# Kernel tuning notes

Measured on AMD Instinct MI355X. Metric: run time of the kernel, lower is better.

## Reference

```python
import jax, jax.numpy as jnp
import numpy as np

D_MODEL = 1024
D_Q = 1024
D_K = 1024
D_V = 1024
B, S = 4, 2048


def setup_inputs() -> dict:
    key = jax.random.key(0)
    kx, kq, kk, kv = jax.random.split(key, 4)
    # torch Linear(in, out) weight is [out, in]; y = x @ W.T. Use kaiming-ish scale.
    sc = 1.0 / np.sqrt(D_MODEL)
    x = jax.random.normal(kx, (B, S, D_MODEL), dtype=jnp.float32)
    Wq = jax.random.normal(kq, (D_Q, D_MODEL), dtype=jnp.float32) * sc
    Wk = jax.random.normal(kk, (D_K, D_MODEL), dtype=jnp.float32) * sc
    Wv = jax.random.normal(kv, (D_V, D_MODEL), dtype=jnp.float32) * sc
    return {"x": x, "Wq": Wq, "Wk": Wk, "Wv": Wv}


def reference(x, Wq, Wk, Wv):
    d_k = Wk.shape[0]
    q = jnp.einsum('bsd,qd->bsq', x, Wq)  # [B,S,d_q]
    k = jnp.einsum('bsd,kd->bsk', x, Wk)  # [B,S,d_k]
    v = jnp.einsum('bsd,vd->bsv', x, Wv)  # [B,S,d_v]
    scores = jnp.einsum('bqd,bkd->bqk', q, k) / jnp.sqrt(jnp.float32(d_k))
    seq = scores.shape[-1]
    causal = jnp.tril(jnp.ones((seq, seq), dtype=bool))  # True = keep
    scores = jnp.where(causal[None, :, :], scores, -jnp.inf)
    probs = jax.nn.softmax(scores, axis=-1)
    return jnp.einsum('bqk,bkv->bqv', probs, v)
```

## Files before the change

kernel.cpp:

```cpp
#include <hip/hip_runtime.h>
#include <hip/hip_bf16.h>
#include <stdint.h>

typedef __attribute__((ext_vector_type(8))) short short8;
typedef __attribute__((ext_vector_type(4))) float floatx4;

typedef const __attribute__((address_space(1))) void* gvp;
typedef __attribute__((address_space(3))) void* lvp;

__device__ __forceinline__ unsigned short f2bf(float f) {
    unsigned u = __float_as_uint(f);
    u += 0x7fffu + ((u >> 16) & 1u);
    return (unsigned short)(u >> 16);
}

#define BAR()   do { asm volatile("" ::: "memory"); __builtin_amdgcn_s_barrier(); asm volatile("" ::: "memory"); } while (0)
#define WAITL() do { asm volatile("s_waitcnt lgkmcnt(0)" ::: "memory"); __builtin_amdgcn_sched_barrier(0); } while (0)
#define WAITV4() asm volatile("s_waitcnt vmcnt(4)" ::: "memory")
#define WAITV0() asm volatile("s_waitcnt vmcnt(0)" ::: "memory")

__global__ __launch_bounds__(256)
void cvt_all(const float* __restrict__ x, const float* __restrict__ wq,
             const float* __restrict__ wk, const float* __restrict__ wv,
             unsigned short* __restrict__ Xb, unsigned short* __restrict__ WqT,
             unsigned short* __restrict__ WkT, unsigned short* __restrict__ Wvb) {
    const int b = blockIdx.x, t = threadIdx.x;
    if (b < 2304) {
        const float* in; unsigned short* out; long base;
        if (b < 2048) { in = x;  out = Xb;  base = (long)b * 1024; }
        else          { in = wv; out = Wvb; base = (long)(b - 2048) * 1024; }
        #pragma unroll
        for (int k = 0; k < 4; ++k) {
            long idx = base + k * 256 + t;
            float4 v = reinterpret_cast<const float4*>(in)[idx];
            uint2 o;
            o.x = (unsigned)f2bf(v.x) | ((unsigned)f2bf(v.y) << 16);
            o.y = (unsigned)f2bf(v.z) | ((unsigned)f2bf(v.w) << 16);
            reinterpret_cast<uint2*>(out)[idx] = o;
        }
    } else {
        const int bb = b - 2304;
        const float* in = (bb < 256) ? wq : wk;
        unsigned short* out = (bb < 256) ? WqT : WkT;
        const int tile = bb & 255;
        const int e0 = (tile >> 4) * 64, d0 = (tile & 15) * 64;
        __shared__ unsigned short ldsT[64][68];
        const int r = t >> 4, cq = t & 15;
        #pragma unroll
        for (int p = 0; p < 4; ++p) {
            const int e = p * 16 + r;
            float4 v = *reinterpret_cast<const float4*>(in + (long)(e0 + e) * 1024 + d0 + cq * 4);
            ldsT[cq*4+0][e] = f2bf(v.x);
            ldsT[cq*4+1][e] = f2bf(v.y);
            ldsT[cq*4+2][e] = f2bf(v.z);
            ldsT[cq*4+3][e] = f2bf(v.w);
        }
        __syncthreads();
        #pragma unroll
        for (int p = 0; p < 4; ++p) {
            const int d = p * 16 + r;
            ushort4 o = *reinterpret_cast<const ushort4*>(&ldsT[d][cq * 4]);
            *reinterpret_cast<ushort4*>(out + (long)(d0 + d) * 1024 + e0 + cq * 4) = o;
        }
    }
}

__device__ __forceinline__ void stage_half(char* slot, const unsigned short* src,
                                           int ld, int k0, int tid) {
    #pragma unroll
    for (int r = 0; r < 2; ++r) {
        const int c = r * 512 + tid;
        const int row = c >> 3;
        const int cs = ((c & 7) * 16) ^ ((row & 7) << 4);
        const char* g = reinterpret_cast<const char*>(src + (long)row * ld + k0) + cs;
        __builtin_amdgcn_global_load_lds((gvp)g,
            (lvp)(slot + r * 8192 + (tid >> 6) * 1024), 16, 0, 0);
    }
}

__device__ __forceinline__ void load_a4(short8 a_[4][2], const char* slot, int mh,
                                        int fr, int csw0, int csw1) {
    #pragma unroll
    for (int i = 0; i < 4; ++i) {
        const int rb = (mh * 64 + i * 16 + fr) * 128;
        a_[i][0] = *reinterpret_cast<const short8*>(slot + rb + csw0);
        a_[i][1] = *reinterpret_cast<const short8*>(slot + rb + csw1);
    }
}

__device__ __forceinline__ void load_b2(short8 b_[2][2], const char* slot, int rbase,
                                        int nh, int fr, int csw0, int csw1) {
    #pragma unroll
    for (int j = 0; j < 2; ++j) {
        const int rb = (rbase + nh * 32 + j * 16 + fr) * 128;
        b_[j][0] = *reinterpret_cast<const short8*>(slot + rb + csw0);
        b_[j][1] = *reinterpret_cast<const short8*>(slot + rb + csw1);
    }
}

__device__ __forceinline__ void mfma16(floatx4 acc[8][4], short8 a_[4][2],
                                       short8 b_[2][2], int mh, int nh) {
    __builtin_amdgcn_s_setprio(1);
    #pragma unroll
    for (int i = 0; i < 4; ++i)
        #pragma unroll
        for (int j = 0; j < 2; ++j) {
            acc[mh*4+i][nh*2+j] = __builtin_amdgcn_mfma_f32_16x16x32_bf16(
                a_[i][0], b_[j][0], acc[mh*4+i][nh*2+j], 0, 0, 0);
            acc[mh*4+i][nh*2+j] = __builtin_amdgcn_mfma_f32_16x16x32_bf16(
                a_[i][1], b_[j][1], acc[mh*4+i][nh*2+j], 0, 0, 0);
        }
    __builtin_amdgcn_s_setprio(0);
}

template<typename CT, int MODE>
__global__ __launch_bounds__(512, 2)
void gemm8p(const unsigned short* __restrict__ A, const unsigned short* B,
            const unsigned short* B1, CT* __restrict__ C, unsigned short* __restrict__ Vt,
            int K, int lda, int ldb, int ldc,
            long sA, long sB, long sC, int nwg)
{
    const int gx = gridDim.x, gy = gridDim.y;
    int flat = (blockIdx.z * gy + blockIdx.y) * gx + blockIdx.x;
    {
        int xcd = flat & 7, lid = flat >> 3;
        int q = nwg >> 3, r = nwg & 7;
        flat = (xcd < r ? xcd * (q + 1) : r * (q + 1) + (xcd - r) * q) + lid;
    }
    int bx, by, bz = 0;
    bool isV = false;
    if (MODE == 1) {
        bx = flat % gx;
        int t2 = flat / gx;
        by = t2 % gy;
        bz = t2 / gy;
        if (bx > by) return;
    } else {
        if (flat >= 128) { isV = true; flat -= 128; B = B1; }
        by = flat >> 2;
        bx = flat & 3;
    }

    A += (long)bz * sA + (long)by * 256 * lda;
    B += (long)bz * sB + (long)bx * 256 * ldb;
    C += (long)bz * sC;

    __shared__ __align__(16) char lds[8 * 16384];
    #define SLOT(db, op, half) (lds + ((((db) << 1 | (op)) << 1 | (half)) * 16384))

    const int tid  = threadIdx.x;
    const int lane = tid & 63;
    const int wid  = tid >> 6;
    const int wm = wid >> 2;
    const int wn = wid & 3;
    const int bh = wn >> 1;
    const int brbase = (wn & 1) * 64;
    const int fr = lane & 15;
    const int csw0 = ((lane >> 4) * 16) ^ ((fr & 7) << 4);
    const int csw1 = (64 + (lane >> 4) * 16) ^ ((fr & 7) << 4);

    const unsigned short* Ah[2] = { A, A + 128ll * lda };
    const unsigned short* Bh[2] = { B, B + 128ll * ldb };

    const int NT = K >> 6;
    const int NI = NT >> 1;

    floatx4 acc[8][4] = {};
    short8 a_[4][2];
    short8 b_[2][2][2];

    stage_half(SLOT(0,1,0), Bh[0], ldb, 0, tid);
    stage_half(SLOT(0,1,1), Bh[1], ldb, 0, tid);
    stage_half(SLOT(0,0,0), Ah[0], lda, 0, tid);
    stage_half(SLOT(0,0,1), Ah[1], lda, 0, tid);
    stage_half(SLOT(1,1,0), Bh[0], ldb, 64, tid);
    stage_half(SLOT(1,1,1), Bh[1], ldb, 64, tid);
    WAITV4();
    BAR();

    for (int I = 0; I < NI; ++I) {
        const int kA1 = min(2*I + 1, NT - 1) * 64;
        const int kT2 = min(2*I + 2, NT - 1) * 64;
        const int kB3 = min(2*I + 3, NT - 1) * 64;

        load_a4(a_, SLOT(0,0,wm), 0, fr, csw0, csw1);
        load_b2(b_[0], SLOT(0,1,bh), brbase, 0, fr, csw0, csw1);
        stage_half(SLOT(1,0,0), Ah[0], lda, kA1, tid);
        BAR(); WAITL();
        mfma16(acc, a_, b_[0], 0, 0);
        BAR();

        load_b2(b_[1], SLOT(0,1,bh), brbase, 1, fr, csw0, csw1);
        stage_half(SLOT(1,0,1), Ah[1], lda, kA1, tid);
        BAR(); WAITL();
        mfma16(acc, a_, b_[1], 0, 1);
        BAR();

        load_a4(a_, SLOT(0,0,wm), 1, fr, csw0, csw1);
        stage_half(SLOT(0,1,0), Bh[0], ldb, kT2, tid);
        BAR(); WAITL();
        mfma16(acc, a_, b_[1], 1, 1);
        BAR();

        stage_half(SLOT(0,1,1), Bh[1], ldb, kT2, tid);
        BAR(); WAITL();
        mfma16(acc, a_, b_[0], 1, 0);
        WAITV4();
        BAR();

        load_a4(a_, SLOT(1,0,wm), 0, fr, csw0, csw1);
        load_b2(b_[0], SLOT(1,1,bh), brbase, 0, fr, csw0, csw1);
        stage_half(SLOT(0,0,0), Ah[0], lda, kT2, tid);
        BAR(); WAITL();
        mfma16(acc, a_, b_[0], 0, 0);
        BAR();

        load_b2(b_[1], SLOT(1,1,bh), brbase, 1, fr, csw0, csw1);
        stage_half(SLOT(0,0,1), Ah[1], lda, kT2, tid);
        BAR(); WAITL();
        mfma16(acc, a_, b_[1], 0, 1);
        BAR();

        load_a4(a_, SLOT(1,0,wm), 1, fr, csw0, csw1);
        stage_half(SLOT(1,1,0), Bh[0], ldb, kB3, tid);
        BAR(); WAITL();
        mfma16(acc, a_, b_[1], 1, 1);
        BAR();

        stage_half(SLOT(1,1,1), Bh[1], ldb, kB3, tid);
        BAR(); WAITL();
        mfma16(acc, a_, b_[0], 1, 0);
        WAITV4();
        BAR();
    }

    if (MODE == 3 && isV) {
        WAITV0();
        BAR();
        char* T = lds;
        #pragma unroll
        for (int i = 0; i < 8; ++i)
            #pragma unroll
            for (int j = 0; j < 4; ++j) {
                const int n = wn * 64 + j * 16 + fr;
                const int m = wm * 128 + ((lane >> 4) << 2) + i * 16;
                uint2 pk;
                pk.x = (unsigned)f2bf(acc[i][j][0]) | ((unsigned)f2bf(acc[i][j][1]) << 16);
                pk.y = (unsigned)f2bf(acc[i][j][2]) | ((unsigned)f2bf(acc[i][j][3]) << 16);
                *reinterpret_cast<uint2*>(T + n * 512 + ((m * 2) ^ ((n & 7) << 4))) = pk;
            }
        __syncthreads();
        const int b  = by >> 3;
        const int s0 = (by & 7) * 256;
        #pragma unroll
        for (int c = 0; c < 16; ++c) {
            const int idx = c * 512 + tid;
            const int n = idx >> 5, k = idx & 31;
            uint4 v = *reinterpret_cast<const uint4*>(T + n * 512 + ((k * 16) ^ ((n & 7) << 4)));
            *reinterpret_cast<uint4*>(Vt + (long)b * (1024 * 2048)
                + (long)(bx * 256 + n) * 2048 + s0 + k * 8) = v;
        }
        return;
    }

    const int cr0 = by * 256 + wm * 128 + (lane >> 4) * 4;
    const int cc0 = bx * 256 + wn * 64 + (lane & 15);
    #pragma unroll
    for (int i = 0; i < 8; ++i)
        #pragma unroll
        for (int j = 0; j < 4; ++j)
            #pragma unroll
            for (int r = 0; r < 4; ++r) {
                long idx = (long)(cr0 + i * 16 + r) * ldc + (cc0 + j * 16);
                float v = acc[i][j][r];
                if constexpr (sizeof(CT) == 4) C[idx] = v;
                else                           C[idx] = (CT)f2bf(v);
            }
    #undef SLOT
}

template<typename CT, int MODE>
__global__ __launch_bounds__(256, 3)
void gemm_bt(const unsigned short* __restrict__ A, const unsigned short* __restrict__ B,
             CT* __restrict__ C, int K, int lda, int ldb, int ldc,
             long sA, long sB, long sC, int nwg, float csc)
{
    const int gx = gridDim.x, gy = gridDim.y;
    int flat = (blockIdx.z * gy + blockIdx.y) * gx + blockIdx.x;
    {
        int xcd = flat & 7, lid = flat >> 3;
        int q = nwg >> 3, r = nwg & 7;
        flat = (xcd < r ? xcd * (q + 1) : r * (q + 1) + (xcd - r) * q) + lid;
    }
    int bx = flat % gx;
    int t2 = flat / gx;
    int by = t2 % gy;
    const int bz = t2 / gy;
    if (MODE == 2) {
        by = ((by & 1) << 3) | ((by & 2) << 1) | ((by & 4) >> 1) | ((by & 8) >> 3);
    }

    A += (long)bz * sA; B += (long)bz * sB; C += (long)bz * sC;
    const int kend = (MODE == 2) ? min(K, (by + 1) * 128) : K;

    __shared__ unsigned short As[128 * 64];
    __shared__ unsigned short Bs[128 * 64];

    const int tid  = threadIdx.x;
    const int lane = tid & 63;
    const int wid  = tid >> 6;
    const int m0 = by * 128, n0 = bx * 128;
    const int wm = (wid >> 1) * 64, wn = (wid & 1) * 64;
    const int frow = lane & 15;
    const int fk   = (lane >> 4) * 8;

    const int srow = lane >> 3;
    const int scolb = (lane & 7) * 16;

    floatx4 acc[4][4] = {};

    for (int k0 = 0; k0 < kend; k0 += 64) {
        __syncthreads();
        #pragma unroll
        for (int i = 0; i < 4; ++i) {
            const int c = wid * 4 + i;
            const int row = c * 8 + srow;
            const char* ga = reinterpret_cast<const char*>(A + (long)(m0 + row) * lda + k0) + scolb;
            __builtin_amdgcn_global_load_lds((gvp)ga,
                (lvp)(reinterpret_cast<char*>(As) + c * 1024), 16, 0, 0);
            const char* gb = reinterpret_cast<const char*>(B + (long)(n0 + row) * ldb + k0) + scolb;
            __builtin_amdgcn_global_load_lds((gvp)gb,
                (lvp)(reinterpret_cast<char*>(Bs) + c * 1024), 16, 0, 0);
        }
        __syncthreads();
        #pragma unroll
        for (int ks = 0; ks < 2; ++ks) {
            short8 af[4], bf[4];
            #pragma unroll
            for (int i = 0; i < 4; ++i) {
                const int ar = wm + i * 16 + frow;
                af[i] = *reinterpret_cast<const short8*>(
                    reinterpret_cast<const char*>(As) + ar * 128 + (ks * 32 + fk) * 2);
                const int br = wn + i * 16 + frow;
                bf[i] = *reinterpret_cast<const short8*>(
                    reinterpret_cast<const char*>(Bs) + br * 128 + (ks * 32 + fk) * 2);
            }
            #pragma unroll
            for (int i = 0; i < 4; ++i)
                #pragma unroll
                for (int j = 0; j < 4; ++j)
                    acc[i][j] = __builtin_amdgcn_mfma_f32_16x16x32_bf16(af[i], bf[j], acc[i][j], 0, 0, 0);
        }
    }

    const int cr0 = m0 + wm + (lane >> 4) * 4;
    const int cc0 = n0 + wn + (lane & 15);
    #pragma unroll
    for (int i = 0; i < 4; ++i)
        #pragma unroll
        for (int j = 0; j < 4; ++j)
            #pragma unroll
            for (int r = 0; r < 4; ++r) {
                long idx = (long)(cr0 + i * 16 + r) * ldc + (cc0 + j * 16);
                float v = acc[i][j][r] * csc;
                if constexpr (sizeof(CT) == 4) C[idx] = v;
                else                           C[idx] = (CT)f2bf(v);
            }
}

__global__ __launch_bounds__(256)
void softmax_causal(float* __restrict__ Sc) {
    const int q = blockIdx.x;
    const int b = blockIdx.y;
    float* row = Sc + ((long)b * 2048 + q) * 2048;
    const int t = threadIdx.x;
    const int lane = t & 63, wid = t >> 6;
    const int kend = (q | 127) + 1;

    float vals[8];
    float mx = -INFINITY;
    #pragma unroll
    for (int i = 0; i < 2; ++i) {
        const int c0 = i * 1024 + t * 4;
        if (c0 <= q) {
            float4 v = *reinterpret_cast<const float4*>(row + c0);
            float tmp[4] = {v.x, v.y, v.z, v.w};
            #pragma unroll
            for (int j = 0; j < 4; ++j) {
                float val = (c0 + j <= q) ? tmp[j] : -INFINITY;
                vals[i * 4 + j] = val;
                mx = fmaxf(mx, val);
            }
        } else {
            vals[i*4+0] = vals[i*4+1] = vals[i*4+2] = vals[i*4+3] = -INFINITY;
        }
    }
    #pragma unroll
    for (int o = 32; o > 0; o >>= 1) mx = fmaxf(mx, __shfl_xor(mx, o));
    __shared__ float rmax[4], rsum[4];
    if (lane == 0) rmax[wid] = mx;
    __syncthreads();
    mx = fmaxf(fmaxf(rmax[0], rmax[1]), fmaxf(rmax[2], rmax[3]));

    float s = 0.f;
    #pragma unroll
    for (int k = 0; k < 8; ++k) {
        float e = __expf(vals[k] - mx);
        vals[k] = e;
        s += e;
    }
    #pragma unroll
    for (int o = 32; o > 0; o >>= 1) s += __shfl_xor(s, o);
    if (lane == 0) rsum[wid] = s;
    __syncthreads();
    s = rsum[0] + rsum[1] + rsum[2] + rsum[3];
    const float inv = 1.f / s;

    unsigned short* orow = reinterpret_cast<unsigned short*>(row);
    #pragma unroll
    for (int i = 0; i < 2; ++i) {
        const int c0 = i * 1024 + t * 4;
        if (c0 < kend) {
            uint2 o;
            o.x = (unsigned)f2bf(vals[i*4+0] * inv) | ((unsigned)f2bf(vals[i*4+1] * inv) << 16);
            o.y = (unsigned)f2bf(vals[i*4+2] * inv) | ((unsigned)f2bf(vals[i*4+3] * inv) << 16);
            *reinterpret_cast<uint2*>(orow + c0) = o;
        }
    }
}

extern "C" void kernel_launch(void* const* d_in, const int* in_sizes, int n_in,
                              void* d_out, int out_size, void* d_ws, size_t ws_size,
                              hipStream_t stream) {
    const float* x  = (const float*)d_in[0];
    const float* Wq = (const float*)d_in[1];
    const float* Wk = (const float*)d_in[2];
    const float* Wv = (const float*)d_in[3];
    float* out = (float*)d_out;

    char* w = (char*)d_ws;
    unsigned short* Xb  = (unsigned short*)(w);
    unsigned short* WqT = (unsigned short*)(w + (16ll << 20));
    unsigned short* WkT = (unsigned short*)(w + (18ll << 20));
    unsigned short* Wvb = (unsigned short*)(w + (20ll << 20));
    unsigned short* Yb  = (unsigned short*)(w + (22ll << 20));
    unsigned short* Gp  = (unsigned short*)(w + (38ll << 20));
    unsigned short* Vt  = (unsigned short*)(w + (70ll << 20));
    float* Sc = (float*)(w + (86ll << 20));

    dim3 blk(256);
    cvt_all<<<2816, blk, 0, stream>>>(x, Wq, Wk, Wv, Xb, WqT, WkT, Wvb);

    gemm_bt<unsigned short, 0><<<dim3(8, 8, 1), blk, 0, stream>>>(
        WkT, WqT, Gp, 1024, 1024, 1024, 1024, 0, 0, 0, 64, 0.03125f);

    gemm8p<unsigned short, 3><<<dim3(256, 1, 1), dim3(512), 0, stream>>>(
        Xb, Gp, Wvb, Yb, Vt, 1024, 1024, 1024, 1024,
        0, 0, 0, 256);

    gemm8p<float, 1><<<dim3(8, 8, 4), dim3(512), 0, stream>>>(
        Yb, Xb, nullptr, Sc, nullptr, 1024, 1024, 1024, 2048,
        2048ll * 1024, 2048ll * 1024, 2048ll * 2048, 256);

    softmax_causal<<<dim3(2048, 4), blk, 0, stream>>>(Sc);

    gemm_bt<float, 2><<<dim3(8, 16, 4), blk, 0, stream>>>(
        (const unsigned short*)Sc, Vt, out, 2048, 4096, 2048, 1024,
        2048ll * 4096, 1024ll * 2048, 2048ll * 1024, 512, 1.0f);
}
```

Baseline: 161.5 us.

## Split-K the Wk^T Wq product, pair causal PV tiles, double-buffer LDS

Replaces the 64-block Wk·Wq Gram GEMM with a 4-way split-K kernel (256 blocks) writing fp32 partials, followed by a reduction kernel that scales and converts to bf16. This targets the poor GPU occupancy of the small GEMM. The causal P·V GEMM is rewritten so each block processes a short and a long row tile (pj and 15-pj) to balance triangular work. Both new kernels use double-buffered, XOR-swizzled LDS staging to overlap loads with MFMA. The split-K adds an extra launch and partial-sum traffic, and the tile pairing halves the P·V grid.

```diff
diff --git a/kernel.cpp b/kernel.cpp
--- a/kernel.cpp
+++ b/kernel.cpp
@@ -62,6 +62,161 @@
             ushort4 o = *reinterpret_cast<const ushort4*>(&ldsT[d][cq * 4]);
             *reinterpret_cast<ushort4*>(out + (long)(d0 + d) * 1024 + e0 + cq * 4) = o;
         }
+    }
+}
+
+__device__ __forceinline__ void stage_tile(unsigned short* Abuf, unsigned short* Bbuf,
+                                           const unsigned short* A, int lda,
+                                           const unsigned short* B, int ldb, int k0,
+                                           int wid, int srow, int piece) {
+    #pragma unroll
+    for (int i = 0; i < 4; ++i) {
+        const int c = wid * 4 + i;
+        const int row = c * 8 + srow;
+        const int cs = (piece * 16) ^ ((row & 7) << 4);
+        __builtin_amdgcn_global_load_lds(
+            (gvp)(reinterpret_cast<const char*>(A + (long)row * lda + k0) + cs),
+            (lvp)(reinterpret_cast<char*>(Abuf) + c * 1024), 16, 0, 0);
+        __builtin_amdgcn_global_load_lds(
+            (gvp)(reinterpret_cast<const char*>(B + (long)row * ldb + k0) + cs),
+            (lvp)(reinterpret_cast<char*>(Bbuf) + c * 1024), 16, 0, 0);
+    }
+}
+
+__device__ __forceinline__ void compute_tile(floatx4 acc[4][4], const unsigned short* As,
+                                             const unsigned short* Bs, int wm, int wn,
+                                             int frow, int lane) {
+    #pragma unroll
+    for (int ks = 0; ks < 2; ++ks) {
+        short8 af[4], bf[4];
+        const int colb = ks * 64 + (lane >> 4) * 16;
+        #pragma unroll
+        for (int i = 0; i < 4; ++i) {
+            const int ar = wm + i * 16 + frow;
+            af[i] = *reinterpret_cast<const short8*>(
+                reinterpret_cast<const char*>(As) + ar * 128 + (colb ^ ((ar & 7) << 4)));
+            const int br = wn + i * 16 + frow;
+            bf[i] = *reinterpret_cast<const short8*>(
+                reinterpret_cast<const char*>(Bs) + br * 128 + (colb ^ ((br & 7) << 4)));
+        }
+        #pragma unroll
+        for (int i = 0; i < 4; ++i)
+            #pragma unroll
+            for (int j = 0; j < 4; ++j)
+                acc[i][j] = __builtin_amdgcn_mfma_f32_16x16x32_bf16(af[i], bf[j], acc[i][j], 0, 0, 0);
+    }
+}
+
+__global__ __launch_bounds__(256, 2)
+void g_chunk(const unsigned short* __restrict__ WkT, const unsigned short* __restrict__ WqT,
+             float* __restrict__ Gw) {
+    const int bx = blockIdx.x, by = blockIdx.y, bz = blockIdx.z;
+    const unsigned short* A = WkT + (long)by * 128 * 1024;
+    const unsigned short* B = WqT + (long)bx * 128 * 1024;
+
+    __shared__ unsigned short As[2][128 * 64];
+    __shared__ unsigned short Bs[2][128 * 64];
+
+    const int tid = threadIdx.x, lane = tid & 63, wid = tid >> 6;
+    const int srow = lane >> 3, piece = lane & 7;
+    const int wm = (wid >> 1) * 64, wn = (wid & 1) * 64, frow = lane & 15;
+
+    floatx4 acc[4][4] = {};
+    const int kbase = bz * 256;
+
+    stage_tile(As[0], Bs[0], A, 1024, B, 1024, kbase, wid, srow, piece);
+    WAITV0(); BAR();
+    int cur = 0;
+    #pragma unroll 1
+    for (int t = 0; t < 4; ++t) {
+        if (t < 3)
+            stage_tile(As[cur ^ 1], Bs[cur ^ 1], A, 1024, B, 1024, kbase + (t + 1) * 64,
+                       wid, srow, piece);
+        compute_tile(acc, As[cur], Bs[cur], wm, wn, frow, lane);
+        WAITV0(); BAR();
+        cur ^= 1;
+    }
+
+    float* Cb = Gw + (long)bz * (1 << 20) + (long)(by * 128) * 1024 + bx * 128;
+    const int cr0 = wm + (lane >> 4) * 4;
+    const int cc0 = wn + (lane & 15);
+    #pragma unroll
+    for (int i = 0; i < 4; ++i)
+        #pragma unroll
+        for (int j = 0; j < 4; ++j)
+            #pragma unroll
+            for (int r = 0; r < 4; ++r)
+                Cb[(long)(cr0 + i * 16 + r) * 1024 + cc0 + j * 16] = acc[i][j][r];
+}
+
+__global__ __launch_bounds__(256)
+void reduce_g(const float* __restrict__ Gw, unsigned short* __restrict__ Gp) {
+    const long i4 = (long)blockIdx.x * 256 + threadIdx.x;
+    const long M4 = (1l << 20) / 4;
+    float4 a = reinterpret_cast<const float4*>(Gw)[i4];
+    float4 b = reinterpret_cast<const float4*>(Gw)[i4 + M4];
+    float4 c = reinterpret_cast<const float4*>(Gw)[i4 + 2 * M4];
+    float4 d = reinterpret_cast<const float4*>(Gw)[i4 + 3 * M4];
+    float sx = (a.x + b.x + c.x + d.x) * 0.03125f;
+    float sy = (a.y + b.y + c.y + d.y) * 0.03125f;
+    float sz = (a.z + b.z + c.z + d.z) * 0.03125f;
+    float sw = (a.w + b.w + c.w + d.w) * 0.03125f;
+    uint2 o;
+    o.x = (unsigned)f2bf(sx) | ((unsigned)f2bf(sy) << 16);
+    o.y = (unsigned)f2bf(sz) | ((unsigned)f2bf(sw) << 16);
+    reinterpret_cast<uint2*>(Gp)[i4] = o;
+}
+
+__global__ __launch_bounds__(256, 2)
+void pv_pair(const unsigned short* __restrict__ P, const unsigned short* __restrict__ Vt,
+             float* __restrict__ out) {
+    int flat = (blockIdx.z * 8 + blockIdx.y) * 8 + blockIdx.x;
+    { int xcd = flat & 7, lid = flat >> 3; flat = xcd * 32 + lid; }
+    const int bx = flat % 8;
+    const int pj = (flat / 8) % 8;
+    const int bz = flat / 64;
+
+    const unsigned short* Pb = P + (long)bz * 2048 * 4096;
+    const unsigned short* Bv = Vt + (long)bz * 1024 * 2048 + (long)(bx * 128) * 2048;
+    float* Cb = out + (long)bz * 2048 * 1024;
+
+    __shared__ unsigned short As[2][128 * 64];
+    __shared__ unsigned short Bs[2][128 * 64];
+
+    const int tid = threadIdx.x, lane = tid & 63, wid = tid >> 6;
+    const int srow = lane >> 3, piece = lane & 7;
+    const int wm = (wid >> 1) * 64, wn = (wid & 1) * 64, frow = lane & 15;
+
+    #pragma unroll 1
+    for (int j = 0; j < 2; ++j) {
+        const int by = j ? 15 - pj : pj;
+        const unsigned short* A = Pb + (long)by * 128 * 4096;
+        const int nt = (by + 1) * 2;
+
+        floatx4 acc[4][4] = {};
+        stage_tile(As[0], Bs[0], A, 4096, Bv, 2048, 0, wid, srow, piece);
+        WAITV0(); BAR();
+        int cur = 0;
+        #pragma unroll 1
+        for (int t = 0; t < nt; ++t) {
+            if (t + 1 < nt)
+                stage_tile(As[cur ^ 1], Bs[cur ^ 1], A, 4096, Bv, 2048, (t + 1) * 64,
+                           wid, srow, piece);
+            compute_tile(acc, As[cur], Bs[cur], wm, wn, frow, lane);
+            WAITV0(); BAR();
+            cur ^= 1;
+        }
+
+        float* Cj = Cb + (long)(by * 128) * 1024 + bx * 128;
+        const int cr0 = wm + (lane >> 4) * 4;
+        const int cc0 = wn + (lane & 15);
+        #pragma unroll
+        for (int i = 0; i < 4; ++i)
+            #pragma unroll
+            for (int jj = 0; jj < 4; ++jj)
+                #pragma unroll
+                for (int r = 0; r < 4; ++r)
+                    Cj[(long)(cr0 + i * 16 + r) * 1024 + cc0 + jj * 16] = acc[i][jj][r];
     }
 }
 
@@ -279,95 +434,6 @@
     #undef SLOT
 }
 
-template<typename CT, int MODE>
-__global__ __launch_bounds__(256, 3)
-void gemm_bt(const unsigned short* __restrict__ A, const unsigned short* __restrict__ B,
-             CT* __restrict__ C, int K, int lda, int ldb, int ldc,
-             long sA, long sB, long sC, int nwg, float csc)
-{
-    const int gx = gridDim.x, gy = gridDim.y;
-    int flat = (blockIdx.z * gy + blockIdx.y) * gx + blockIdx.x;
-    {
-        int xcd = flat & 7, lid = flat >> 3;
-        int q = nwg >> 3, r = nwg & 7;
-        flat = (xcd < r ? xcd * (q + 1) : r * (q + 1) + (xcd - r) * q) + lid;
-    }
-    int bx = flat % gx;
-    int t2 = flat / gx;
-    int by = t2 % gy;
-    const int bz = t2 / gy;
-    if (MODE == 2) {
-        by = ((by & 1) << 3) | ((by & 2) << 1) | ((by & 4) >> 1) | ((by & 8) >> 3);
-    }
-
-    A += (long)bz * sA; B += (long)bz * sB; C += (long)bz * sC;
-    const int kend = (MODE == 2) ? min(K, (by + 1) * 128) : K;
-
-    __shared__ unsigned short As[128 * 64];
-    __shared__ unsigned short Bs[128 * 64];
-
-    const int tid  = threadIdx.x;
-    const int lane = tid & 63;
-    const int wid  = tid >> 6;
-    const int m0 = by * 128, n0 = bx * 128;
-    const int wm = (wid >> 1) * 64, wn = (wid & 1) * 64;
-    const int frow = lane & 15;
-    const int fk   = (lane >> 4) * 8;
-
-    const int srow = lane >> 3;
-    const int scolb = (lane & 7) * 16;
-
-    floatx4 acc[4][4] = {};
-
-    for (int k0 = 0; k0 < kend; k0 += 64) {
-        __syncthreads();
-        #pragma unroll
-        for (int i = 0; i < 4; ++i) {
-            const int c = wid * 4 + i;
-            const int row = c * 8 + srow;
-            const char* ga = reinterpret_cast<const char*>(A + (long)(m0 + row) * lda + k0) + scolb;
-            __builtin_amdgcn_global_load_lds((gvp)ga,
-                (lvp)(reinterpret_cast<char*>(As) + c * 1024), 16, 0, 0);
-            const char* gb = reinterpret_cast<const char*>(B + (long)(n0 + row) * ldb + k0) + scolb;
-            __builtin_amdgcn_global_load_lds((gvp)gb,
-                (lvp)(reinterpret_cast<char*>(Bs) + c * 1024), 16, 0, 0);
-        }
-        __syncthreads();
-        #pragma unroll
-        for (int ks = 0; ks < 2; ++ks) {
-            short8 af[4], bf[4];
-            #pragma unroll
-            for (int i = 0; i < 4; ++i) {
-                const int ar = wm + i * 16 + frow;
-                af[i] = *reinterpret_cast<const short8*>(
-                    reinterpret_cast<const char*>(As) + ar * 128 + (ks * 32 + fk) * 2);
-                const int br = wn + i * 16 + frow;
-                bf[i] = *reinterpret_cast<const short8*>(
-                    reinterpret_cast<const char*>(Bs) + br * 128 + (ks * 32 + fk) * 2);
-            }
-            #pragma unroll
-            for (int i = 0; i < 4; ++i)
-                #pragma unroll
-                for (int j = 0; j < 4; ++j)
-                    acc[i][j] = __builtin_amdgcn_mfma_f32_16x16x32_bf16(af[i], bf[j], acc[i][j], 0, 0, 0);
-        }
-    }
-
-    const int cr0 = m0 + wm + (lane >> 4) * 4;
-    const int cc0 = n0 + wn + (lane & 15);
-    #pragma unroll
-    for (int i = 0; i < 4; ++i)
-        #pragma unroll
-        for (int j = 0; j < 4; ++j)
-            #pragma unroll
-            for (int r = 0; r < 4; ++r) {
-                long idx = (long)(cr0 + i * 16 + r) * ldc + (cc0 + j * 16);
-                float v = acc[i][j][r] * csc;
-                if constexpr (sizeof(CT) == 4) C[idx] = v;
-                else                           C[idx] = (CT)f2bf(v);
-            }
-}
-
 __global__ __launch_bounds__(256)
 void softmax_causal(float* __restrict__ Sc) {
     const int q = blockIdx.x;
@@ -445,14 +511,15 @@
     unsigned short* Wvb = (unsigned short*)(w + (20ll << 20));
     unsigned short* Yb  = (unsigned short*)(w + (22ll << 20));
     unsigned short* Gp  = (unsigned short*)(w + (38ll << 20));
+    float*          Gw  = (float*)(w + (40ll << 20));
     unsigned short* Vt  = (unsigned short*)(w + (70ll << 20));
     float* Sc = (float*)(w + (86ll << 20));
 
     dim3 blk(256);
     cvt_all<<<2816, blk, 0, stream>>>(x, Wq, Wk, Wv, Xb, WqT, WkT, Wvb);
 
-    gemm_bt<unsigned short, 0><<<dim3(8, 8, 1), blk, 0, stream>>>(
-        WkT, WqT, Gp, 1024, 1024, 1024, 1024, 0, 0, 0, 64, 0.03125f);
+    g_chunk<<<dim3(8, 8, 4), blk, 0, stream>>>(WkT, WqT, Gw);
+    reduce_g<<<1024, blk, 0, stream>>>(Gw, Gp);
 
     gemm8p<unsigned short, 3><<<dim3(256, 1, 1), dim3(512), 0, stream>>>(
         Xb, Gp, Wvb, Yb, Vt, 1024, 1024, 1024, 1024,
@@ -464,7 +531,5 @@
 
     softmax_causal<<<dim3(2048, 4), blk, 0, stream>>>(Sc);
 
-    gemm_bt<float, 2><<<dim3(8, 16, 4), blk, 0, stream>>>(
-        (const unsigned short*)Sc, Vt, out, 2048, 4096, 2048, 1024,
-        2048ll * 4096, 1024ll * 2048, 2048ll * 1024, 512, 1.0f);
-}
+    pv_pair<<<dim3(8, 8, 4), blk, 0, stream>>>((const unsigned short*)Sc, Vt, out);
+}
```

Result: faster. 145.3 us (-10.0%).
